# Kernel optimization log

Measured on AMD Instinct MI355X. Metric: run time of the kernel, lower is better.

The kernel has to match this reference:

```python
import jax, jax.numpy as jnp
import numpy as np
import math

STRIDE = ((2, 2), (4, 4), (8, 8), (16, 16))  # (ws, hs) pairs
D_MODEL = 256
B, H, W = 8, 128, 128
BN_EPS = 1e-5
LEAKY_SLOPE = 0.2


def setup_inputs() -> dict:
    key = jax.random.key(0)
    ks = jax.random.split(key, 8)
    s = 1.0 / math.sqrt(D_MODEL)
    s3 = 1.0 / math.sqrt(D_MODEL * 9)
    return {
        "x": jax.random.normal(ks[0], (B, D_MODEL, H, W), jnp.float32),
        "wq": jax.random.normal(ks[1], (D_MODEL, D_MODEL, 1, 1), jnp.float32) * s,
        "bq": jnp.zeros((D_MODEL,), jnp.float32),
        "wk": jax.random.normal(ks[2], (D_MODEL, D_MODEL, 1, 1), jnp.float32) * s,
        "bk": jnp.zeros((D_MODEL,), jnp.float32),
        "wv": jax.random.normal(ks[3], (D_MODEL, D_MODEL, 1, 1), jnp.float32) * s,
        "bv": jnp.zeros((D_MODEL,), jnp.float32),
        "wo": jax.random.normal(ks[4], (D_MODEL, D_MODEL, 3, 3), jnp.float32) * s3,
        "bo": jnp.zeros((D_MODEL,), jnp.float32),
        "gamma": jnp.ones((D_MODEL,), jnp.float32),
        "beta": jnp.zeros((D_MODEL,), jnp.float32),
    }


def _conv1x1(x, w, bias):
    # 1x1 conv == channel matmul
    return jnp.einsum('bchw,oc->bohw', x, w[:, :, 0, 0]) + bias[None, :, None, None]


def reference(x, wq, bq, wk, bk, wv, bv, wo, bo, gamma, beta):
    b, c, h, w = x.shape
    n = len(STRIDE)
    d_k = c // n
    q = _conv1x1(x, wq, bq)
    k = _conv1x1(x, wk, bk)
    v = _conv1x1(x, wv, bv)
    outs = []
    for idx, (ws, hs) in enumerate(STRIDE):
        lo = idx * d_k
        oh, ow = h // hs, w // ws

        def gather(t):
            # strided patch gather: element (i,j) head <- t[:, :, i::hs, j::ws]
            t = t[:, lo:lo + d_k].reshape(b, d_k, oh, hs, ow, ws)
            return t.transpose(0, 3, 5, 1, 2, 4).reshape(b, hs * ws, d_k * oh * ow)

        qi, ki, vi = gather(q), gather(k), gather(v)
        scale = 1.0 / jnp.sqrt(jnp.asarray(qi.shape[-1], qi.dtype))
        scores = jnp.einsum('bsd,btd->bst', qi, ki) * scale  # [b, hs*ws, hs*ws]
        p = jax.nn.softmax(scores, axis=-1)
        y = jnp.einsum('bst,btd->bsd', p, vi)
        # scatter back exactly as the torch permute(0,3,1,4,2,5): h = i*oh + row
        y = y.reshape(b, hs, ws, d_k, oh, ow).transpose(0, 3, 1, 4, 2, 5).reshape(b, d_k, h, w)
        outs.append(y)
    out = jnp.concatenate(outs, axis=1)  # [b, c, h, w]
    # output_linear: 3x3 conv -> BatchNorm2d (training-mode batch stats) -> LeakyReLU(0.2)
    out = jax.lax.conv_general_dilated(out, wo, (1, 1), 'SAME',
                                       dimension_numbers=('NCHW', 'OIHW', 'NCHW'))
    out = out + bo[None, :, None, None]
    mean = out.mean(axis=(0, 2, 3))
    var = out.var(axis=(0, 2, 3))
    out = (out - mean[None, :, None, None]) * jax.lax.rsqrt(var[None, :, None, None] + BN_EPS)
    out = out * gamma[None, :, None, None] + beta[None, :, None, None]
    return jnp.where(out > 0, out, LEAKY_SLOPE * out)
```

## Files before the change

kernel.cpp:

```cpp
#include <hip/hip_runtime.h>
#include <stdint.h>


#define DEVI static __device__ __forceinline__

typedef short bf8 __attribute__((ext_vector_type(8)));
typedef float f32x4 __attribute__((ext_vector_type(4)));

DEVI unsigned short f2bf(float f) {
  unsigned u = __builtin_bit_cast(unsigned, f);
  u = (u + 0x7fffu + ((u >> 16) & 1u)) >> 16;
  return (unsigned short)u;
}
DEVI float bf2f(unsigned short h) {
  unsigned u = ((unsigned)h) << 16;
  return __builtin_bit_cast(float, u);
}

DEVI void gload16(const void* g, void* l) {
  __builtin_amdgcn_global_load_lds(
      (const __attribute__((address_space(1))) unsigned int*)g,
      (__attribute__((address_space(3))) unsigned int*)l, 16, 0, 0);
}

static const size_t WB_OFF  = 0;
static const size_t WOB_OFF = 393216;
static const size_t QN_OFF  = 1572864;
static const size_t KN_OFF  = QN_OFF + 67108864;
static const size_t VN_OFF  = KN_OFF + 67108864;
static const size_t YN_OFF  = VN_OFF + 67108864;
static const size_t SC_OFF  = YN_OFF + 67108864;
static const size_t PRB_OFF = SC_OFF + 2236928;
static const size_t BNP_OFF = PRB_OFF + 1118464;
static const size_t BNS_OFF = BNP_OFF + 4194304;
static const size_t ZP_OFF  = BNS_OFF + 2048;
static const size_t WS_NEED = ZP_OFF + 256;

__global__ void k_prep(const float* __restrict__ wq, const float* __restrict__ wk,
                       const float* __restrict__ wv, const float* __restrict__ wo,
                       unsigned short* __restrict__ Wb, unsigned short* __restrict__ Wob) {
  int i = blockIdx.x * 256 + threadIdx.x;
  if (i < 196608) {
    int z = i >> 16, r = i & 65535;
    const float* w = (z == 0) ? wq : (z == 1) ? wk : wv;
    Wb[i] = f2bf(w[r]);
  } else {
    int j = i - 196608;
    int o = j / 2304, k = j - o * 2304;
    int e = k >> 8, c = k & 255;
    Wob[j] = f2bf(wo[(o * 256 + c) * 9 + e]);
  }
}

__global__ void k_zero(float* __restrict__ p, int n) {
  int i = blockIdx.x * 256 + threadIdx.x;
  for (; i < n; i += gridDim.x * 256) p[i] = 0.f;
}

__global__ __launch_bounds__(256) void k_qkv(
    const float* __restrict__ x, const unsigned short* __restrict__ Wb,
    const float* __restrict__ bq, const float* __restrict__ bk, const float* __restrict__ bv,
    unsigned short* __restrict__ Qn, unsigned short* __restrict__ Kn,
    unsigned short* __restrict__ Vn) {
  const int pt = blockIdx.x, b = blockIdx.y;
  const int p0 = pt * 64;
  const int tid = threadIdx.x;

  __shared__ __align__(16) unsigned short xt[64 * 256];
  __shared__ __align__(16) unsigned short ot[64 * 256];

  const float* xb = x + (size_t)b * 256 * 16384;
  for (int k = 0; k < 16; ++k) {
    int i = tid + k * 256;
    int c = i >> 4, p4 = (i & 15) * 4;
    float4 v = *(const float4*)(xb + (size_t)c * 16384 + p0 + p4);
    xt[(p4 + 0) * 256 + (c ^ (((p4 + 0) & 7) << 3))] = f2bf(v.x);
    xt[(p4 + 1) * 256 + (c ^ (((p4 + 1) & 7) << 3))] = f2bf(v.y);
    xt[(p4 + 2) * 256 + (c ^ (((p4 + 2) & 7) << 3))] = f2bf(v.z);
    xt[(p4 + 3) * 256 + (c ^ (((p4 + 3) & 7) << 3))] = f2bf(v.w);
  }
  __syncthreads();

  const int wave = tid >> 6, lane = tid & 63;
  const int lr = lane & 15, lk = lane >> 4;
  const int obase = wave * 64;

  for (int z = 0; z < 3; ++z) {
    const unsigned short* Wz = Wb + (size_t)z * 65536;
    f32x4 acc[4][4];
    for (int m = 0; m < 4; ++m)
      for (int n = 0; n < 4; ++n)
        for (int r = 0; r < 4; ++r) acc[m][n][r] = 0.f;

    for (int ks = 0; ks < 8; ++ks) {
      int c0 = ks * 32 + lk * 8;
      bf8 a[4], bb[4];
#pragma unroll
      for (int m = 0; m < 4; ++m)
        a[m] = *(const bf8*)(Wz + (size_t)(obase + m * 16 + lr) * 256 + c0);
#pragma unroll
      for (int n = 0; n < 4; ++n) {
        int p = n * 16 + lr;
        bb[n] = *(const bf8*)(&xt[p * 256 + (c0 ^ ((p & 7) << 3))]);
      }
#pragma unroll
      for (int m = 0; m < 4; ++m)
#pragma unroll
        for (int n = 0; n < 4; ++n)
          acc[m][n] = __builtin_amdgcn_mfma_f32_16x16x32_bf16(a[m], bb[n], acc[m][n], 0, 0, 0);
    }

    const float* bias = (z == 0) ? bq : (z == 1) ? bk : bv;
    unsigned short* On = (z == 0) ? Qn : (z == 1) ? Kn : Vn;
    __syncthreads();
#pragma unroll
    for (int m = 0; m < 4; ++m) {
      int ob4 = obase + m * 16 + lk * 4;
      float4 b4 = *(const float4*)(bias + ob4);
#pragma unroll
      for (int n = 0; n < 4; ++n) {
        int p = n * 16 + lr;
        ushort4 v4;
        v4.x = f2bf(acc[m][n][0] + b4.x);
        v4.y = f2bf(acc[m][n][1] + b4.y);
        v4.z = f2bf(acc[m][n][2] + b4.z);
        v4.w = f2bf(acc[m][n][3] + b4.w);
        *(ushort4*)(&ot[p * 256 + (ob4 ^ ((p & 7) << 3))]) = v4;
      }
    }
    __syncthreads();
    unsigned short* gb = On + ((size_t)b * 16384 + p0) * 256;
#pragma unroll
    for (int i = 0; i < 8; ++i) {
      int ch = tid + i * 256;
      *(uint4*)(gb + ch * 8) = *(const uint4*)(&ot[ch * 8]);
    }
  }
}

template <int IDX>
__global__ __launch_bounds__(256) void k_gram(
    const unsigned short* __restrict__ Qn, const unsigned short* __restrict__ Kn,
    float* __restrict__ scores) {
  constexpr int HS = 2 << IDX, S = HS * HS, OH = 64 >> IDX, NSP = OH * OH;
  constexpr int SPW = (IDX == 2) ? 2 : 8;
  constexpr int DSUB = SPW * 64;
  constexpr int SPB = NSP / 32;
  constexpr int STEPS = SPB / SPW;
  constexpr int ROWS = S;
  constexpr int TPT = S * SPW * 8 / 256;
  constexpr int SCOFF = (IDX == 0) ? 0 : (IDX == 1) ? 128 : 2176;
  constexpr int HC = IDX * 64;
  constexpr int MT = (IDX == 2) ? 4 : 1;

  const int chk = blockIdx.x, b = blockIdx.y;
  const int tid = threadIdx.x;
  const int wave = tid >> 6, lane = tid & 63, lr = lane & 15, lk = lane >> 4;

  __shared__ __align__(16) unsigned short qg[ROWS * DSUB];
  __shared__ __align__(16) unsigned short kg[ROWS * DSUB];
  __shared__ float red[S * S];

  const size_t base = (size_t)b * 16384 * 256;

  f32x4 acc[MT][MT];
  for (int m = 0; m < MT; ++m)
    for (int n = 0; n < MT; ++n)
      for (int r = 0; r < 4; ++r) acc[m][n][r] = 0.f;

  for (int st = 0; st < STEPS; ++st) {
    const int sp0 = chk * SPB + st * SPW;
    __syncthreads();
#pragma unroll
    for (int r = 0; r < TPT; ++r) {
      int task = tid + r * 256;
      int cg = task & 7, pl = task >> 3;
      int spl = pl >> (2 * (IDX + 1)), s = pl & (S - 1);
      int sp = sp0 + spl;
      int ohi = sp >> (6 - IDX), owi = sp & (OH - 1);
      int ii = s >> (IDX + 1), jj = s & (HS - 1);
      int p = (ohi * HS + ii) * 128 + owi * HS + jj;
      size_t gaddr = base + (size_t)p * 256 + HC + ((cg ^ (p & 7)) << 3);
      int laddr = s * DSUB + (((spl * 8 + cg) ^ (s & 7)) << 3);
      *(uint4*)(qg + laddr) = *(const uint4*)(Qn + gaddr);
      *(uint4*)(kg + laddr) = *(const uint4*)(Kn + gaddr);
    }
    __syncthreads();
    if (IDX == 2) {
      int kgid = wave * 4 + lk;
      bf8 a[4], bb[4];
#pragma unroll
      for (int m = 0; m < 4; ++m) {
        int row = m * 16 + lr;
        int off = row * DSUB + ((kgid ^ (row & 7)) << 3);
        a[m] = *(const bf8*)(qg + off);
        bb[m] = *(const bf8*)(kg + off);
      }
#pragma unroll
      for (int m = 0; m < 4; ++m)
#pragma unroll
        for (int n = 0; n < 4; ++n)
          acc[m][n] = __builtin_amdgcn_mfma_f32_16x16x32_bf16(a[m], bb[n], acc[m][n], 0, 0, 0);
    } else {
      int row = lr & (ROWS - 1);
#pragma unroll
      for (int kk = 0; kk < 4; ++kk) {
        int kgid = (wave * 4 + kk) * 4 + lk;
        int off = row * DSUB + ((kgid ^ (row & 7)) << 3);
        bf8 a = *(const bf8*)(qg + off);
        bf8 bb = *(const bf8*)(kg + off);
        acc[0][0] = __builtin_amdgcn_mfma_f32_16x16x32_bf16(a, bb, acc[0][0], 0, 0, 0);
      }
    }
  }

  __syncthreads();
  for (int i2 = tid; i2 < S * S; i2 += 256) red[i2] = 0.f;
  __syncthreads();
  if (IDX == 2) {
#pragma unroll
    for (int m = 0; m < 4; ++m)
#pragma unroll
      for (int n = 0; n < 4; ++n)
#pragma unroll
        for (int r = 0; r < 4; ++r)
          atomicAdd(&red[(m * 16 + lk * 4 + r) * 64 + n * 16 + lr], acc[m][n][r]);
  } else if (IDX == 1) {
#pragma unroll
    for (int r = 0; r < 4; ++r)
      atomicAdd(&red[(lk * 4 + r) * 16 + lr], acc[0][0][r]);
  } else {
    if (lk == 0 && lr < 4) {
#pragma unroll
      for (int r = 0; r < 4; ++r)
        atomicAdd(&red[r * 4 + lr], acc[0][0][r]);
    }
  }
  __syncthreads();
  float* sc = scores + SCOFF + (size_t)b * S * S;
  for (int i2 = tid; i2 < S * S; i2 += 256) atomicAdd(sc + i2, red[i2]);
}

__global__ __launch_bounds__(256) void k_gram3(
    const unsigned short* __restrict__ Qn, const unsigned short* __restrict__ Kn,
    float* __restrict__ part3) {
  const int qc = blockIdx.x, tq = blockIdx.y, b = blockIdx.z;
  const int tid = threadIdx.x;
  const int wave = tid >> 6, lane = tid & 63, lr = lane & 15, lk = lane >> 4;

  __shared__ __align__(16) unsigned short qg[256 * 64];
  __shared__ __align__(16) unsigned short kg[64 * 64];

  const size_t base = (size_t)b * 16384 * 256;

  f32x4 acc[4][4];
  for (int m = 0; m < 4; ++m)
    for (int n = 0; n < 4; ++n)
      for (int r = 0; r < 4; ++r) acc[m][n][r] = 0.f;

  for (int st = 0; st < 8; ++st) {
    int sp = qc * 8 + st;
    int ohi = sp >> 3, owi = sp & 7;
    __syncthreads();
#pragma unroll
    for (int r = 0; r < 8; ++r) {
      int task = tid + r * 256;
      int cg = task & 7, s = task >> 3;
      int p = (ohi * 16 + (s >> 4)) * 128 + owi * 16 + (s & 15);
      uint4 v = *(const uint4*)(Qn + base + (size_t)p * 256 + 192 + ((cg ^ (p & 7)) << 3));
      *(uint4*)(qg + s * 64 + ((cg ^ (s & 7)) << 3)) = v;
    }
#pragma unroll
    for (int r = 0; r < 2; ++r) {
      int task = tid + r * 256;
      int cg = task & 7, tl = task >> 3;
      int p = (ohi * 16 + tq * 4 + (tl >> 4)) * 128 + owi * 16 + (tl & 15);
      uint4 v = *(const uint4*)(Kn + base + (size_t)p * 256 + 192 + ((cg ^ (p & 7)) << 3));
      *(uint4*)(kg + tl * 64 + ((cg ^ (tl & 7)) << 3)) = v;
    }
    __syncthreads();
#pragma unroll
    for (int kk = 0; kk < 2; ++kk) {
      int kgid = kk * 4 + lk;
      bf8 a[4], bb[4];
#pragma unroll
      for (int m = 0; m < 4; ++m) {
        int row = wave * 64 + m * 16 + lr;
        a[m] = *(const bf8*)(qg + row * 64 + ((kgid ^ (row & 7)) << 3));
      }
#pragma unroll
      for (int n = 0; n < 4; ++n) {
        int rowb = n * 16 + lr;
        bb[n] = *(const bf8*)(kg + rowb * 64 + ((kgid ^ (rowb & 7)) << 3));
      }
#pragma unroll
      for (int m = 0; m < 4; ++m)
#pragma unroll
        for (int n = 0; n < 4; ++n)
          acc[m][n] = __builtin_amdgcn_mfma_f32_16x16x32_bf16(a[m], bb[n], acc[m][n], 0, 0, 0);
    }
  }

  float* pb = part3 + (((size_t)qc * 8 + b) * 65536);
#pragma unroll
  for (int m = 0; m < 4; ++m)
#pragma unroll
    for (int r = 0; r < 4; ++r) {
      int srow = wave * 64 + m * 16 + lk * 4 + r;
#pragma unroll
      for (int n = 0; n < 4; ++n)
        pb[srow * 256 + tq * 64 + n * 16 + lr] = acc[m][n][r];
    }
}

__global__ __launch_bounds__(256) void k_softmax(const float* __restrict__ scores,
                                                 unsigned short* __restrict__ prb) {
  const int idx = blockIdx.x, b = blockIdx.y;
  const int S = 4 << (2 * idx);
  const int off = (idx == 0 ? 0 : idx == 1 ? 128 : 2176) + b * S * S;
  const int s = threadIdx.x;
  if (s >= S) return;
  const float scale = rsqrtf(64.0f * (float)(4096 >> (2 * idx)));
  const float* row = scores + off + s * S;
  float m = -1e30f;
  for (int t = 0; t < S; ++t) m = fmaxf(m, row[t]);
  m *= scale;
  float sum = 0.f;
  for (int t = 0; t < S; ++t) sum += __expf(row[t] * scale - m);
  float inv = 1.0f / sum;
  unsigned short* prow = prb + off + s * S;
  for (int t = 0; t < S; ++t) prow[t] = f2bf(__expf(row[t] * scale - m) * inv);
}

__global__ __launch_bounds__(256) void k_softmax3(const float* __restrict__ part3,
                                                  unsigned short* __restrict__ prb) {
  const int sc_ = blockIdx.x, b = blockIdx.y;
  const int tid = threadIdx.x;
  const int s = sc_ * 32 + (tid >> 3);
  const int t0 = (tid & 7) * 32;
  float v[32];
#pragma unroll
  for (int k = 0; k < 32; ++k) v[k] = 0.f;
  for (int q = 0; q < 8; ++q) {
    const float4* pp = (const float4*)(part3 + (((size_t)q * 8 + b) * 256 + s) * 256 + t0);
#pragma unroll
    for (int k = 0; k < 8; ++k) {
      float4 u = pp[k];
      v[k * 4 + 0] += u.x; v[k * 4 + 1] += u.y; v[k * 4 + 2] += u.z; v[k * 4 + 3] += u.w;
    }
  }
  const float scale = 1.0f / 64.0f;
  float m = -1e30f;
#pragma unroll
  for (int k = 0; k < 32; ++k) { v[k] *= scale; m = fmaxf(m, v[k]); }
  m = fmaxf(m, __shfl_xor(m, 1));
  m = fmaxf(m, __shfl_xor(m, 2));
  m = fmaxf(m, __shfl_xor(m, 4));
  float sum = 0.f;
#pragma unroll
  for (int k = 0; k < 32; ++k) { v[k] = __expf(v[k] - m); sum += v[k]; }
  sum += __shfl_xor(sum, 1);
  sum += __shfl_xor(sum, 2);
  sum += __shfl_xor(sum, 4);
  float inv = 1.0f / sum;
  unsigned short* prw = prb + 34944 + (size_t)b * 65536 + s * 256 + t0;
#pragma unroll
  for (int k8 = 0; k8 < 4; ++k8) {
    unsigned short tmp[8];
#pragma unroll
    for (int e = 0; e < 8; ++e) tmp[e] = f2bf(v[k8 * 8 + e] * inv);
    *(uint4*)(prw + k8 * 8) = *(const uint4*)tmp;
  }
}

template <int IDX>
__global__ __launch_bounds__(256) void k_pv(
    const unsigned short* __restrict__ Vn, const unsigned short* __restrict__ prb,
    unsigned short* __restrict__ Yn) {
  constexpr int HS = 2 << IDX, S = HS * HS, OH = 64 >> IDX;
  constexpr int IT = (IDX == 0) ? 8 : (IDX == 1) ? 4 : 1;
  constexpr int POFF = (IDX == 0) ? 0 : (IDX == 1) ? 128 : 2176;
  const int bx = blockIdx.x, b = blockIdx.y;
  const int c = threadIdx.x & 63, spg = threadIdx.x >> 6;
  __shared__ __align__(16) float pl[S * S];
  const unsigned short* pr = prb + POFF + (size_t)b * S * S;
  for (int i = threadIdx.x; i < S * S; i += 256) pl[i] = bf2f(pr[i]);
  __syncthreads();
  const int hc = IDX * 64;
  const unsigned short* vb = Vn + (size_t)b * 16384 * 256;
  unsigned short* yb = Yn + (size_t)b * 16384 * 256;
  for (int it = 0; it < IT; ++it) {
    int sp = bx * (4 * IT) + it * 4 + spg;
    int ohi = sp >> (6 - IDX), owi = sp & (OH - 1);
    float v[S];
#pragma unroll
    for (int t = 0; t < S; ++t) {
      int po = (ohi * HS + t / HS) * 128 + owi * HS + (t % HS);
      v[t] = bf2f(vb[(size_t)po * 256 + ((hc + c) ^ ((po & 7) << 3))]);
    }
    for (int s = 0; s < S; ++s) {
      const float4* p4 = (const float4*)(pl + s * S);
      float a = 0.f;
#pragma unroll
      for (int t4 = 0; t4 < S / 4; ++t4) {
        float4 pp = p4[t4];
        a += pp.x * v[t4 * 4] + pp.y * v[t4 * 4 + 1] + pp.z * v[t4 * 4 + 2] + pp.w * v[t4 * 4 + 3];
      }
      int po = ((s >> (IDX + 1)) * OH + ohi) * 128 + (s & (HS - 1)) * OH + owi;
      yb[(size_t)po * 256 + ((hc + c) ^ ((po & 7) << 3))] = f2bf(a);
    }
  }
}

__global__ __launch_bounds__(256) void k_pv3(
    const unsigned short* __restrict__ Vn, const unsigned short* __restrict__ prb,
    unsigned short* __restrict__ Yn) {
  const int sp = blockIdx.x, b = blockIdx.y;
  const int ohi = sp >> 3, owi = sp & 7;
  const int tid = threadIdx.x;
  __shared__ __align__(16) unsigned short vl[64 * 256];
  const unsigned short* vb = Vn + (size_t)b * 16384 * 256;
  {
    int t = tid;
    int po = (ohi * 16 + (t >> 4)) * 128 + owi * 16 + (t & 15);
    const unsigned short* src = vb + (size_t)po * 256;
    int xv = (po & 7) << 3;
#pragma unroll
    for (int g = 0; g < 8; ++g) {
      ushort4 lo = *(const ushort4*)(src + ((192 + g * 8) ^ xv));
      ushort4 hi = *(const ushort4*)(src + ((192 + g * 8) ^ xv) + 4);
      unsigned short vv[8] = {lo.x, lo.y, lo.z, lo.w, hi.x, hi.y, hi.z, hi.w};
#pragma unroll
      for (int e = 0; e < 8; ++e) {
        int cc = g * 8 + e;
        vl[cc * 256 + (t ^ ((cc & 7) << 3))] = vv[e];
      }
    }
  }
  __syncthreads();

  const int wave = tid >> 6, lane = tid & 63;
  const int lr = lane & 15, lk = lane >> 4;
  const int sb = wave * 64;
  const unsigned short* pr = prb + 34944 + (size_t)b * 65536;

  f32x4 acc[4][4];
  for (int m = 0; m < 4; ++m)
    for (int n = 0; n < 4; ++n)
      for (int r = 0; r < 4; ++r) acc[m][n][r] = 0.f;

  for (int kk = 0; kk < 8; ++kk) {
    int t0 = kk * 32 + lk * 8;
    bf8 a[4], bb[4];
#pragma unroll
    for (int m = 0; m < 4; ++m)
      a[m] = *(const bf8*)(pr + (size_t)(sb + m * 16 + lr) * 256 + t0);
#pragma unroll
    for (int n = 0; n < 4; ++n) {
      int cc = n * 16 + lr;
      bb[n] = *(const bf8*)(&vl[cc * 256 + (t0 ^ ((cc & 7) << 3))]);
    }
#pragma unroll
    for (int m = 0; m < 4; ++m)
#pragma unroll
      for (int n = 0; n < 4; ++n)
        acc[m][n] = __builtin_amdgcn_mfma_f32_16x16x32_bf16(a[m], bb[n], acc[m][n], 0, 0, 0);
  }

  unsigned short* yb = Yn + (size_t)b * 16384 * 256;
#pragma unroll
  for (int m = 0; m < 4; ++m) {
#pragma unroll
    for (int r = 0; r < 4; ++r) {
      int s = sb + m * 16 + lk * 4 + r;
      int si = s >> 4, sj = s & 15;
      int po = (si * 8 + ohi) * 128 + sj * 8 + owi;
#pragma unroll
      for (int n = 0; n < 4; ++n) {
        int cc = 192 + n * 16 + lr;
        yb[(size_t)po * 256 + (cc ^ (owi << 3))] = f2bf(acc[m][n][r]);
      }
    }
  }
}

#define CONV_PHASE(KT_, R_, PK_, DOSTAGE_, WAITMODE_)                            \
  do {                                                                           \
    if (DOSTAGE_) {                                                              \
      constexpr int type_ = (R_ == 0) ? 0 : (R_ == 1) ? 2 : (R_ == 2) ? 3 : 1;   \
      STAGE((1 - (PK_)) * 4 + (R_), type_, (KT_) + 1);                           \
    }                                                                            \
    if ((WAITMODE_) == 0) { asm volatile("s_waitcnt vmcnt(6)" ::: "memory"); }   \
    else if ((WAITMODE_) == 1) { asm volatile("s_waitcnt vmcnt(0)" ::: "memory"); } \
    __builtin_amdgcn_s_barrier();                                                \
    asm volatile("" ::: "memory");                                               \
    {                                                                            \
      constexpr int mh_ = (R_) >> 1, nh_ = (R_) & 1;                             \
      constexpr int sA_ = (PK_) * 4 + (mh_ ? 3 : 0);                             \
      constexpr int sB_ = (PK_) * 4 + (nh_ ? 2 : 1);                             \
      if (nh_ == 0) {                                                            \
        _Pragma("unroll") for (int m2 = 0; m2 < 4; ++m2) {                       \
          int row = wm * 64 + m2 * 16 + lr;                                      \
          _Pragma("unroll") for (int kk = 0; kk < 2; ++kk)                       \
            areg[m2][kk] = *(const bf8*)(&lds[sA_][row * 64 +                    \
                (((kk * 4 + lk) ^ (row & 7)) << 3)]);                            \
        }                                                                        \
      }                                                                          \
      bf8 breg[2][2];                                                            \
      _Pragma("unroll") for (int n2 = 0; n2 < 2; ++n2) {                         \
        int row = wn * 32 + n2 * 16 + lr;                                        \
        _Pragma("unroll") for (int kk = 0; kk < 2; ++kk)                         \
          breg[n2][kk] = *(const bf8*)(&lds[sB_][row * 64 +                      \
              (((kk * 4 + lk) ^ (row & 7)) << 3)]);                              \
      }                                                                          \
      __builtin_amdgcn_s_setprio(1);                                             \
      _Pragma("unroll") for (int kk = 0; kk < 2; ++kk)                           \
        _Pragma("unroll") for (int m2 = 0; m2 < 4; ++m2)                         \
          _Pragma("unroll") for (int n2 = 0; n2 < 2; ++n2)                       \
            acc[mh_ * 4 + m2][nh_ * 2 + n2] =                                    \
                __builtin_amdgcn_mfma_f32_16x16x32_bf16(                         \
                    areg[m2][kk], breg[n2][kk],                                  \
                    acc[mh_ * 4 + m2][nh_ * 2 + n2], 0, 0, 0);                   \
      __builtin_amdgcn_s_setprio(0);                                             \
      asm volatile("" ::: "memory");                                             \
    }                                                                            \
  } while (0)

__global__ __launch_bounds__(512, 2) void k_conv(
    const unsigned short* __restrict__ Yn, const unsigned short* __restrict__ Wob,
    const float* __restrict__ bo, const unsigned short* __restrict__ zp,
    unsigned short* __restrict__ co, float* __restrict__ bnp) {
  __shared__ __align__(16) unsigned short lds[8][8192];

  const int bid = blockIdx.x;
  const int swz = (bid & 7) * 64 + (bid >> 3);
  const int b = swz >> 6, tile = swz & 63;
  const int y0 = (tile >> 3) * 16, x0 = (tile & 7) * 16;
  const int tid = threadIdx.x;
  const int wave = tid >> 6, lane = tid & 63;
  const int lr = lane & 15, lk = lane >> 4;
  const int wm = wave >> 2, wn = wave & 3;
  const int cg = lane & 7;

  const unsigned short* yb = Yn + (size_t)b * 16384 * 256;

  auto STAGE = [&](int slot, int type, int KT) {
    if (type < 2) {
      const unsigned short* wsrc = Wob + (KT >> 2) * 256 + (KT & 3) * 64;
#pragma unroll
      for (int j = 0; j < 2; ++j) {
        int rp = (wave * 2 + j) * 8 + (lane >> 3);
        int o = ((rp >> 6) & 1) * 128 + type * 64 + (rp & 63);
        int kg = cg ^ (rp & 7);
        gload16(wsrc + o * 2304 + (kg << 3), &lds[slot][(wave * 2 + j) * 512]);
      }
    } else {
      int e = KT >> 2;
      int dy = e / 3 - 1, dx = e % 3 - 1, c8 = (KT & 3) * 8;
#pragma unroll
      for (int j = 0; j < 2; ++j) {
        int rp = (wave * 2 + j) * 8 + (lane >> 3);
        int n = ((rp >> 5) & 3) * 64 + (type - 2) * 32 + (rp & 31);
        int kg = cg ^ (rp & 7);
        int h = y0 + (n >> 4) + dy, ww = x0 + (n & 15) + dx;
        const unsigned short* src = zp;
        if (h >= 0 && h < 128 && ww >= 0 && ww < 128) {
          int pp = h * 128 + ww;
          src = yb + (size_t)pp * 256 + ((c8 + (kg ^ (pp & 7))) << 3);
        }
        gload16(src, &lds[slot][(wave * 2 + j) * 512]);
      }
    }
  };

  f32x4 acc[8][4];
#pragma unroll
  for (int m = 0; m < 8; ++m)
#pragma unroll
    for (int n = 0; n < 4; ++n)
#pragma unroll
      for (int r = 0; r < 4; ++r) acc[m][n][r] = 0.f;

  bf8 areg[4][2];

  STAGE(0, 0, 0); STAGE(1, 2, 0); STAGE(2, 3, 0); STAGE(3, 1, 0);
  asm volatile("s_waitcnt vmcnt(0)" ::: "memory");

  for (int gg = 0; gg < 17; ++gg) {
    const int k0 = gg * 2;
    CONV_PHASE(k0, 0, 0, true, 0);
    CONV_PHASE(k0, 1, 0, true, 0);
    CONV_PHASE(k0, 2, 0, true, 0);
    CONV_PHASE(k0, 3, 0, true, 0);
    CONV_PHASE(k0 + 1, 0, 1, true, 0);
    CONV_PHASE(k0 + 1, 1, 1, true, 0);
    CONV_PHASE(k0 + 1, 2, 1, true, 0);
    CONV_PHASE(k0 + 1, 3, 1, true, 0);
  }
  CONV_PHASE(34, 0, 0, true, 0);
  CONV_PHASE(34, 1, 0, true, 0);
  CONV_PHASE(34, 2, 0, true, 0);
  CONV_PHASE(34, 3, 0, true, 0);
  CONV_PHASE(35, 0, 1, false, 1);
  CONV_PHASE(35, 1, 1, false, 2);
  CONV_PHASE(35, 2, 1, false, 2);
  CONV_PHASE(35, 3, 1, false, 2);

  __syncthreads();
  unsigned short* cb = co + (size_t)b * 256 * 16384;
  float* red1 = (float*)&lds[0][0];
  float* red2 = red1 + 1024;
#pragma unroll
  for (int m = 0; m < 8; ++m) {
#pragma unroll
    for (int r = 0; r < 4; ++r) {
      int o = wm * 128 + m * 16 + lk * 4 + r;
      float bvv = bo[o];
      float s1 = 0.f, s2 = 0.f;
#pragma unroll
      for (int n = 0; n < 4; ++n) {
        int pix = wn * 64 + n * 16 + lr;
        int py = pix >> 4, px = pix & 15;
        float v = acc[m][n][r] + bvv;
        cb[(size_t)o * 16384 + (y0 + py) * 128 + x0 + px] = f2bf(v);
        s1 += v;
        s2 += v * v;
      }
      for (int off = 1; off < 16; off <<= 1) {
        s1 += __shfl_xor(s1, off, 64);
        s2 += __shfl_xor(s2, off, 64);
      }
      if (lr == 0) {
        int ol = m * 16 + lk * 4 + r;
        red1[wave * 128 + ol] = s1;
        red2[wave * 128 + ol] = s2;
      }
    }
  }
  __syncthreads();
  {
    int o = tid & 255, stat = tid >> 8;
    int wm2 = o >> 7, ol = o & 127;
    const float* rd = stat ? red2 : red1;
    float s = rd[(wm2 * 4 + 0) * 128 + ol] + rd[(wm2 * 4 + 1) * 128 + ol] +
              rd[(wm2 * 4 + 2) * 128 + ol] + rd[(wm2 * 4 + 3) * 128 + ol];
    bnp[((size_t)(b * 64 + tile) * 256 + o) * 2 + stat] = s;
  }
}

__global__ __launch_bounds__(256) void k_bnred(
    const float* __restrict__ bnp, const float* __restrict__ gamma,
    const float* __restrict__ beta, float* __restrict__ bns) {
  const int o = blockIdx.x;
  const int tid = threadIdx.x;
  float s1 = 0.f, s2 = 0.f;
  for (int k = tid; k < 512; k += 256) {
    s1 += bnp[((size_t)k * 256 + o) * 2 + 0];
    s2 += bnp[((size_t)k * 256 + o) * 2 + 1];
  }
  __shared__ float r1[256], r2[256];
  r1[tid] = s1; r2[tid] = s2;
  __syncthreads();
  for (int off = 128; off > 0; off >>= 1) {
    if (tid < off) { r1[tid] += r1[tid + off]; r2[tid] += r2[tid + off]; }
    __syncthreads();
  }
  if (tid == 0) {
    const float cnt = 8.0f * 16384.0f;
    float mean = r1[0] / cnt;
    float var = r2[0] / cnt - mean * mean;
    float sc = gamma[o] * rsqrtf(var + 1e-5f);
    bns[o] = sc;
    bns[256 + o] = beta[o] - mean * sc;
  }
}

__global__ void k_bnapply(const unsigned short* __restrict__ co, float* __restrict__ out,
                          const float* __restrict__ bns) {
  size_t i = ((size_t)blockIdx.x * 256 + threadIdx.x) * 8;
  const size_t total = 33554432;
  const size_t stride = (size_t)gridDim.x * 256 * 8;
  for (; i < total; i += stride) {
    uint4 v = *(const uint4*)(co + i);
    int o = (int)((i >> 14) & 255);
    float sc = bns[o], shv = bns[256 + o];
    const unsigned short* pv = (const unsigned short*)&v;
    float r[8];
#pragma unroll
    for (int e = 0; e < 8; ++e) {
      float f = bf2f(pv[e]) * sc + shv;
      r[e] = f > 0.f ? f : 0.2f * f;
    }
    *(float4*)(out + i) = *(const float4*)&r[0];
    *(float4*)(out + i + 4) = *(const float4*)&r[4];
  }
}

extern "C" void kernel_launch(void* const* d_in, const int* in_sizes, int n_in,
                              void* d_out, int out_size, void* d_ws, size_t ws_size,
                              hipStream_t stream) {
  if (ws_size < WS_NEED) return;

  const float* x     = (const float*)d_in[0];
  const float* wq    = (const float*)d_in[1];
  const float* bq    = (const float*)d_in[2];
  const float* wk    = (const float*)d_in[3];
  const float* bk    = (const float*)d_in[4];
  const float* wv    = (const float*)d_in[5];
  const float* bv    = (const float*)d_in[6];
  const float* wo    = (const float*)d_in[7];
  const float* bo    = (const float*)d_in[8];
  const float* gamma = (const float*)d_in[9];
  const float* beta  = (const float*)d_in[10];
  float* out = (float*)d_out;
  char* ws = (char*)d_ws;

  unsigned short* Wb  = (unsigned short*)(ws + WB_OFF);
  unsigned short* Wob = (unsigned short*)(ws + WOB_OFF);
  unsigned short* Qn  = (unsigned short*)(ws + QN_OFF);
  unsigned short* Kn  = (unsigned short*)(ws + KN_OFF);
  unsigned short* Vn  = (unsigned short*)(ws + VN_OFF);
  unsigned short* Yn  = (unsigned short*)(ws + YN_OFF);
  float* part3 = (float*)(ws + YN_OFF);
  unsigned short* co = (unsigned short*)(ws + QN_OFF);
  float* scores = (float*)(ws + SC_OFF);
  unsigned short* prb = (unsigned short*)(ws + PRB_OFF);
  float* bnp    = (float*)(ws + BNP_OFF);
  float* bns    = (float*)(ws + BNS_OFF);
  unsigned short* zp = (unsigned short*)(ws + ZP_OFF);

  k_prep<<<dim3(3072), dim3(256), 0, stream>>>(wq, wk, wv, wo, Wb, Wob);
  k_zero<<<dim3(137), dim3(256), 0, stream>>>(scores, 34944);
  k_zero<<<dim3(1), dim3(64), 0, stream>>>((float*)zp, 64);
  k_qkv<<<dim3(256, 8), dim3(256), 0, stream>>>(x, Wb, bq, bk, bv, Qn, Kn, Vn);
  k_gram<0><<<dim3(32, 8), dim3(256), 0, stream>>>(Qn, Kn, scores);
  k_gram<1><<<dim3(32, 8), dim3(256), 0, stream>>>(Qn, Kn, scores);
  k_gram<2><<<dim3(32, 8), dim3(256), 0, stream>>>(Qn, Kn, scores);
  k_gram3<<<dim3(8, 4, 8), dim3(256), 0, stream>>>(Qn, Kn, part3);
  k_softmax<<<dim3(3, 8), dim3(256), 0, stream>>>(scores, prb);
  k_softmax3<<<dim3(8, 8), dim3(256), 0, stream>>>(part3, prb);
  k_pv<0><<<dim3(128, 8), dim3(256), 0, stream>>>(Vn, prb, Yn);
  k_pv<1><<<dim3(64, 8), dim3(256), 0, stream>>>(Vn, prb, Yn);
  k_pv<2><<<dim3(64, 8), dim3(256), 0, stream>>>(Vn, prb, Yn);
  k_pv3<<<dim3(64, 8), dim3(256), 0, stream>>>(Vn, prb, Yn);
  k_conv<<<dim3(512), dim3(512), 0, stream>>>(Yn, Wob, bo, zp, co, bnp);
  k_bnred<<<dim3(256), dim3(256), 0, stream>>>(bnp, gamma, beta, bns);
  k_bnapply<<<dim3(4096), dim3(256), 0, stream>>>(co, out, bns);
}
```

Measured before the change: 571.1 us.

## Retile QKV projection to 256-pixel blocks with 512 threads and chunked epilogue

```diff
diff --git a/kernel.cpp b/kernel.cpp
--- a/kernel.cpp
+++ b/kernel.cpp
@@ -57,83 +57,105 @@
   for (; i < n; i += gridDim.x * 256) p[i] = 0.f;
 }
 
-__global__ __launch_bounds__(256) void k_qkv(
+__global__ __launch_bounds__(512, 2) void k_qkv(
     const float* __restrict__ x, const unsigned short* __restrict__ Wb,
     const float* __restrict__ bq, const float* __restrict__ bk, const float* __restrict__ bv,
     unsigned short* __restrict__ Qn, unsigned short* __restrict__ Kn,
     unsigned short* __restrict__ Vn) {
+  __shared__ __align__(16) unsigned short xs[256 * 256];
+  __shared__ __align__(16) unsigned short ot[32 * 256];
+
   const int pt = blockIdx.x, b = blockIdx.y;
-  const int p0 = pt * 64;
+  const int p0 = pt * 256;
   const int tid = threadIdx.x;
-
-  __shared__ __align__(16) unsigned short xt[64 * 256];
-  __shared__ __align__(16) unsigned short ot[64 * 256];
-
-  const float* xb = x + (size_t)b * 256 * 16384;
-  for (int k = 0; k < 16; ++k) {
-    int i = tid + k * 256;
-    int c = i >> 4, p4 = (i & 15) * 4;
-    float4 v = *(const float4*)(xb + (size_t)c * 16384 + p0 + p4);
-    xt[(p4 + 0) * 256 + (c ^ (((p4 + 0) & 7) << 3))] = f2bf(v.x);
-    xt[(p4 + 1) * 256 + (c ^ (((p4 + 1) & 7) << 3))] = f2bf(v.y);
-    xt[(p4 + 2) * 256 + (c ^ (((p4 + 2) & 7) << 3))] = f2bf(v.z);
-    xt[(p4 + 3) * 256 + (c ^ (((p4 + 3) & 7) << 3))] = f2bf(v.w);
-  }
-  __syncthreads();
-
   const int wave = tid >> 6, lane = tid & 63;
   const int lr = lane & 15, lk = lane >> 4;
-  const int obase = wave * 64;
+  const int wm = wave >> 2, wn = wave & 3;
+
+  const float* xb = x + (size_t)b * 256 * 16384 + p0;
+#pragma unroll
+  for (int i = 0; i < 16; ++i) {
+    int task = tid + i * 512;
+    int p = task & 255, g = task >> 8;
+    unsigned short tmp[8];
+#pragma unroll
+    for (int e = 0; e < 8; ++e)
+      tmp[e] = f2bf(xb[(size_t)(g * 8 + e) * 16384 + p]);
+    *(uint4*)(&xs[p * 256 + ((g ^ (p & 7)) << 3)]) = *(const uint4*)tmp;
+  }
+  __syncthreads();
 
   for (int z = 0; z < 3; ++z) {
     const unsigned short* Wz = Wb + (size_t)z * 65536;
-    f32x4 acc[4][4];
-    for (int m = 0; m < 4; ++m)
-      for (int n = 0; n < 4; ++n)
-        for (int r = 0; r < 4; ++r) acc[m][n][r] = 0.f;
-
-    for (int ks = 0; ks < 8; ++ks) {
-      int c0 = ks * 32 + lk * 8;
-      bf8 a[4], bb[4];
-#pragma unroll
-      for (int m = 0; m < 4; ++m)
-        a[m] = *(const bf8*)(Wz + (size_t)(obase + m * 16 + lr) * 256 + c0);
-#pragma unroll
-      for (int n = 0; n < 4; ++n) {
-        int p = n * 16 + lr;
-        bb[n] = *(const bf8*)(&xt[p * 256 + (c0 ^ ((p & 7) << 3))]);
-      }
-#pragma unroll
-      for (int m = 0; m < 4; ++m)
-#pragma unroll
-        for (int n = 0; n < 4; ++n)
-          acc[m][n] = __builtin_amdgcn_mfma_f32_16x16x32_bf16(a[m], bb[n], acc[m][n], 0, 0, 0);
-    }
-
     const float* bias = (z == 0) ? bq : (z == 1) ? bk : bv;
     unsigned short* On = (z == 0) ? Qn : (z == 1) ? Kn : Vn;
-    __syncthreads();
-#pragma unroll
-    for (int m = 0; m < 4; ++m) {
-      int ob4 = obase + m * 16 + lk * 4;
-      float4 b4 = *(const float4*)(bias + ob4);
+
+    f32x4 acc[8][4];
+#pragma unroll
+    for (int m = 0; m < 8; ++m)
+#pragma unroll
+      for (int n = 0; n < 4; ++n)
+#pragma unroll
+        for (int r = 0; r < 4; ++r) acc[m][n][r] = 0.f;
+
+    for (int kt = 0; kt < 4; ++kt) {
+      bf8 a[8][2], bb[4][2];
+#pragma unroll
+      for (int m = 0; m < 8; ++m) {
+        int row = wm * 128 + m * 16 + lr;
+#pragma unroll
+        for (int kk = 0; kk < 2; ++kk)
+          a[m][kk] = *(const bf8*)(Wz + (size_t)row * 256 + kt * 64 + kk * 32 + lk * 8);
+      }
 #pragma unroll
       for (int n = 0; n < 4; ++n) {
-        int p = n * 16 + lr;
-        ushort4 v4;
-        v4.x = f2bf(acc[m][n][0] + b4.x);
-        v4.y = f2bf(acc[m][n][1] + b4.y);
-        v4.z = f2bf(acc[m][n][2] + b4.z);
-        v4.w = f2bf(acc[m][n][3] + b4.w);
-        *(ushort4*)(&ot[p * 256 + (ob4 ^ ((p & 7) << 3))]) = v4;
-      }
-    }
-    __syncthreads();
-    unsigned short* gb = On + ((size_t)b * 16384 + p0) * 256;
-#pragma unroll
-    for (int i = 0; i < 8; ++i) {
-      int ch = tid + i * 256;
-      *(uint4*)(gb + ch * 8) = *(const uint4*)(&ot[ch * 8]);
+        int p = wn * 64 + n * 16 + lr;
+#pragma unroll
+        for (int kk = 0; kk < 2; ++kk) {
+          int g = kt * 8 + kk * 4 + lk;
+          bb[n][kk] = *(const bf8*)(&xs[p * 256 + ((g ^ (p & 7)) << 3)]);
+        }
+      }
+#pragma unroll
+      for (int kk = 0; kk < 2; ++kk)
+#pragma unroll
+        for (int m = 0; m < 8; ++m)
+#pragma unroll
+          for (int n = 0; n < 4; ++n)
+            acc[m][n] = __builtin_amdgcn_mfma_f32_16x16x32_bf16(a[m][kk], bb[n][kk],
+                                                                acc[m][n], 0, 0, 0);
+    }
+
+    for (int pc = 0; pc < 8; ++pc) {
+      if (wn == (pc >> 1)) {
+        const int nsel = (pc & 1) * 2;
+#pragma unroll
+        for (int m = 0; m < 8; ++m) {
+          int o4 = wm * 128 + m * 16 + lk * 4;
+          float4 b4 = *(const float4*)(bias + o4);
+#pragma unroll
+          for (int nn = 0; nn < 2; ++nn) {
+            int n = nsel + nn;
+            int pch = nn * 16 + lr;
+            ushort4 v4;
+            v4.x = f2bf(acc[m][n][0] + b4.x);
+            v4.y = f2bf(acc[m][n][1] + b4.y);
+            v4.z = f2bf(acc[m][n][2] + b4.z);
+            v4.w = f2bf(acc[m][n][3] + b4.w);
+            *(ushort4*)(&ot[pch * 256 + (o4 ^ ((pch & 7) << 3))]) = v4;
+          }
+        }
+      }
+      __syncthreads();
+      {
+        unsigned short* gb = On + ((size_t)b * 16384 + p0 + pc * 32) * 256;
+#pragma unroll
+        for (int i = 0; i < 2; ++i) {
+          int idx = tid + i * 512;
+          *(uint4*)(gb + idx * 8) = *(const uint4*)(&ot[idx * 8]);
+        }
+      }
+      __syncthreads();
     }
   }
 }
@@ -732,7 +754,7 @@
   k_prep<<<dim3(3072), dim3(256), 0, stream>>>(wq, wk, wv, wo, Wb, Wob);
   k_zero<<<dim3(137), dim3(256), 0, stream>>>(scores, 34944);
   k_zero<<<dim3(1), dim3(64), 0, stream>>>((float*)zp, 64);
-  k_qkv<<<dim3(256, 8), dim3(256), 0, stream>>>(x, Wb, bq, bk, bv, Qn, Kn, Vn);
+  k_qkv<<<dim3(64, 8), dim3(512), 0, stream>>>(x, Wb, bq, bk, bv, Qn, Kn, Vn);
   k_gram<0><<<dim3(32, 8), dim3(256), 0, stream>>>(Qn, Kn, scores);
   k_gram<1><<<dim3(32, 8), dim3(256), 0, stream>>>(Qn, Kn, scores);
   k_gram<2><<<dim3(32, 8), dim3(256), 0, stream>>>(Qn, Kn, scores);
```

Result: slower. 710.8 us (+24.5%).
